# Kernel optimization log

Hardware: AMD Instinct MI355X
Metric: run time of the kernel (lower is better)

## Reference

```python
import jax, jax.numpy as jnp
import numpy as np

INF = 1e9  # large finite sentinel (avoid inf arithmetic in potentials)


def _hungarian(cost):
    """Exact linear sum assignment (Jonker-Volgenant style shortest augmenting
    path, O(N^3)) on a single [N, N] cost matrix. Returns col_ind (int32 [N])
    such that row i is matched to column col_ind[i] with minimal total cost
    (same solution as scipy.optimize.linear_sum_assignment up to ties).
    Column index n is a virtual 'start' column (e-maxx formulation)."""
    n = cost.shape[0]

    def row_body(i, carry):
        u, v, p = carry  # u: row potentials [n]; v: col potentials [n+1]; p[j]: row assigned to col j (-1 free)
        p = p.at[n].set(i)
        state = (u, v, p,
                 jnp.full(n + 1, INF, cost.dtype),   # minv
                 jnp.zeros(n + 1, dtype=bool),       # used
                 jnp.zeros(n + 1, dtype=jnp.int32),  # way (parent col on path)
                 jnp.int32(n))                       # j0 current col

        def cond(st):
            _, _, p_, _, _, _, j0 = st
            return p_[j0] >= 0  # stop when we reach a free column

        def body(st):
            u_, v_, p_, minv, used, way, j0 = st
            used = used.at[j0].set(True)
            i0 = p_[j0]
            cur = cost[i0] - u_[i0] - v_[:n]          # reduced costs of row i0 [n]
            cur = jnp.where(used[:n], INF, cur)
            better = cur < minv[:n]
            minv = minv.at[:n].set(jnp.where(better, cur, minv[:n]))
            way = way.at[:n].set(jnp.where(better, j0, way[:n]))
            masked = jnp.where(used[:n], INF, minv[:n])
            j1 = jnp.argmin(masked).astype(jnp.int32)
            delta = masked[j1]
            # dual update: used cols raise row potential, others shrink minv
            u_ = u_.at[p_].add(jnp.where(used, delta, jnp.zeros((), cost.dtype)))
            v_ = jnp.where(used, v_ - delta, v_)
            minv = jnp.where(used, minv, minv - delta)
            return (u_, v_, p_, minv, used, way, j1)

        u, v, p, _, _, way, j0 = jax.lax.while_loop(cond, body, state)

        # augment along the alternating path back to the virtual column
        def cond2(s):
            j, _ = s
            return j != n

        def body2(s):
            j, p_ = s
            j_prev = way[j]
            return j_prev, p_.at[j].set(p_[j_prev])

        _, p = jax.lax.while_loop(cond2, body2, (j0, p))
        return (u, v, p)

    u0 = jnp.zeros(n, cost.dtype)
    v0 = jnp.zeros(n + 1, cost.dtype)
    p0 = jnp.full(n + 1, -1, dtype=jnp.int32)
    _, _, p = jax.lax.fori_loop(0, n, row_body, (u0, v0, p0))
    # p[j] = row matched to col j  ->  col_ind[row] = j
    col_ind = jnp.zeros(n, jnp.int32).at[p[:n]].set(jnp.arange(n, dtype=jnp.int32))
    return col_ind


def setup_inputs() -> dict:
    key = jax.random.key(0)
    k1, k2 = jax.random.split(key)
    B, N, D = 2048, 24, 256
    slots = jax.random.normal(k1, (B, N, D), dtype=jnp.float32)
    prev_slots = jax.random.normal(k2, (B, N, D), dtype=jnp.float32)
    return {"slots": slots, "prev_slots": prev_slots}


def reference(slots, prev_slots):
    """HungarianPredictor.forward with similarity='cosine': reorder current
    slots to align with prev_slots ordering via optimal 1-1 matching."""
    eps = 1e-12  # torch F.normalize eps
    pn = prev_slots / jnp.maximum(
        jnp.linalg.norm(prev_slots, axis=-1, keepdims=True), eps)
    cn = slots / jnp.maximum(
        jnp.linalg.norm(slots, axis=-1, keepdims=True), eps)
    # cost[b, i, j] = 1 - <prev_i, curr_j>   [B, N, N]
    cost = 1.0 - jnp.einsum('bnd,bmd->bnm', pn, cn)
    col = jax.vmap(_hungarian)(jax.lax.stop_gradient(cost))  # [B, N] int32
    reordered = jax.vmap(lambda s, c: s[c])(slots, col)       # gather per batch
    return reordered
```

## Files before the change

### kernel.cpp

```cpp
#include <hip/hip_runtime.h>

#define N 24
#define D 256
#define DP 260
#define CP 26
#define BLK 256
#define NB 4
#define INFV 1e9f

__global__ __launch_bounds__(BLK) void hungarian_fused(
    const float* __restrict__ slots,
    const float* __restrict__ prev,
    float* __restrict__ out, int B)
{
    __shared__ float sp[N][DP];
    __shared__ float sc[N][DP];
    __shared__ float cost[NB][N][CP];
    __shared__ float inrm[2][N];
    __shared__ int   colw[NB][N];

    const int tid  = threadIdx.x;
    const int lane = tid & 63;
    const int wv   = tid >> 6;
    const int b0   = blockIdx.x * NB;

    for (int m = 0; m < NB; ++m) {
        int b = b0 + m;
        if (b < B) {
            const float4* sb4 = (const float4*)(slots + (size_t)b * N * D);
            const float4* pb4 = (const float4*)(prev  + (size_t)b * N * D);
            #pragma unroll
            for (int r = 0; r < 6; ++r) {
                int i = r * 4 + wv;
                float4 a = sb4[i * 64 + lane];
                float4 c = pb4[i * 64 + lane];
                *(float4*)&sc[i][lane * 4] = a;
                *(float4*)&sp[i][lane * 4] = c;
                float sa = a.x*a.x + a.y*a.y + a.z*a.z + a.w*a.w;
                float sb = c.x*c.x + c.y*c.y + c.z*c.z + c.w*c.w;
                #pragma unroll
                for (int off = 32; off >= 1; off >>= 1) {
                    sa += __shfl_xor(sa, off);
                    sb += __shfl_xor(sb, off);
                }
                if (lane == 0) {
                    inrm[1][i] = 1.0f / fmaxf(sqrtf(sa), 1e-12f);
                    inrm[0][i] = 1.0f / fmaxf(sqrtf(sb), 1e-12f);
                }
            }
        }
        __syncthreads();
        if (b < B && tid < 144) {
            int ti = (tid / 12) * 2;
            int tj = (tid % 12) * 2;
            const float4* p0 = (const float4*)&sp[ti][0];
            const float4* p1 = (const float4*)&sp[ti + 1][0];
            const float4* c0 = (const float4*)&sc[tj][0];
            const float4* c1 = (const float4*)&sc[tj + 1][0];
            float a00 = 0.f, a01 = 0.f, a10 = 0.f, a11 = 0.f;
            int q0 = tid & 63;
            #pragma unroll 4
            for (int k = 0; k < 64; ++k) {
                int q = (q0 + k) & 63;
                float4 x0 = p0[q], x1 = p1[q], y0 = c0[q], y1 = c1[q];
                a00 += x0.x*y0.x + x0.y*y0.y + x0.z*y0.z + x0.w*y0.w;
                a01 += x0.x*y1.x + x0.y*y1.y + x0.z*y1.z + x0.w*y1.w;
                a10 += x1.x*y0.x + x1.y*y0.y + x1.z*y0.z + x1.w*y0.w;
                a11 += x1.x*y1.x + x1.y*y1.y + x1.z*y1.z + x1.w*y1.w;
            }
            float rp0 = inrm[0][ti], rp1 = inrm[0][ti + 1];
            float rc0 = inrm[1][tj], rc1 = inrm[1][tj + 1];
            cost[m][ti][tj]         = 1.0f - a00 * (rp0 * rc0);
            cost[m][ti][tj + 1]     = 1.0f - a01 * (rp0 * rc1);
            cost[m][ti + 1][tj]     = 1.0f - a10 * (rp1 * rc0);
            cost[m][ti + 1][tj + 1] = 1.0f - a11 * (rp1 * rc1);
        }
        __syncthreads();
    }

    const int bw = b0 + wv;
    if (bw < B) {
        const int   jl = lane & 31;
        const float* C = &cost[wv][0][0];
        float u = 0.f;
        float v = 0.f;
        int   p = -1;
        const int jc = (jl < N) ? jl : 0;

        for (int i = 0; i < N; ++i) {
            if (jl == N) p = i;
            float minv = INFV;
            int   way  = 0;
            bool  used = false;
            bool  rowInTree = false;
            int   j0 = N;
            int   i0 = i;

            while (true) {
                used       = used       || (jl == j0);
                rowInTree  = rowInTree  || (jl == i0);
                float u_i0 = __shfl(u, i0, 32);
                float cur  = C[i0 * CP + jc] - u_i0 - v;
                bool  active = (jl < N) && !used;
                if (active && cur < minv) { minv = cur; way = j0; }
                float masked = active ? minv : INFV;

                unsigned k = __float_as_uint(masked);
                k = k ^ ((unsigned)(((int)k) >> 31) | 0x80000000u);
                k = (k & 0xFFFFFFE0u) | (unsigned)jl;
                #pragma unroll
                for (int off = 16; off >= 1; off >>= 1) {
                    unsigned o = __shfl_xor(k, off, 32);
                    k = (o < k) ? o : k;
                }
                int   j1    = (int)(k & 31u);
                float delta = __shfl(masked, j1, 32);

                if (jl < N && rowInTree) u += delta;
                if (jl <= N) {
                    if (used) v -= delta; else minv -= delta;
                }
                j0 = j1;
                i0 = __shfl(p, j0, 32);
                if (i0 < 0) break;
            }

            int j = j0;
            while (j != N) {
                int jp  = __shfl(way, j, 32);
                int pjp = __shfl(p, jp, 32);
                if (jl == j) p = pjp;
                j = jp;
            }
        }
        if (lane < 32 && jl < N) colw[wv][p] = jl;
    }

    if (bw < B) {
        const float4* sg4 = (const float4*)(slots + (size_t)bw * N * D);
        float4*       og4 = (float4*)(out + (size_t)bw * N * D);
        #pragma unroll
        for (int i = 0; i < N; ++i) {
            int c = colw[wv][i];
            og4[i * 64 + lane] = sg4[c * 64 + lane];
        }
    }
}

extern "C" void kernel_launch(void* const* d_in, const int* in_sizes, int n_in,
                              void* d_out, int out_size, void* d_ws, size_t ws_size,
                              hipStream_t stream) {
    const float* slots = (const float*)d_in[0];
    const float* prev  = (const float*)d_in[1];
    float* out = (float*)d_out;
    int B = in_sizes[0] / (N * D);
    int grid = (B + NB - 1) / NB;
    hungarian_fused<<<grid, BLK, 0, stream>>>(slots, prev, out, B);
}
```

Before: 209.6 us.

## Rewrite as per-wave Hungarian with register cost rows, greedy init, DPP reductions

Each wave now builds its own batch's cost matrix. Lanes compute a 3x3 tile of dot products straight from global memory, so the shared staging of slots and prev and the block-wide barriers are gone. The transposed cost is loaded into per-lane registers, and a column-reduction plus greedy initial matching pre-assigns rows, so only the remaining free rows need augmenting paths. The argmin uses DPP row operations and readlane instead of shuffles. This removes LDS traffic and syncs, but the 24-way switch and the greedy init add complexity, and the code relies on a wave-local lgkmcnt wait in place of a barrier for correctness.

Result: faster. 194.5 us (-7.2%).

```diff
diff --git a/kernel.cpp b/kernel.cpp
--- a/kernel.cpp
+++ b/kernel.cpp
@@ -1,149 +1,190 @@
 #include <hip/hip_runtime.h>
-
-#define N 24
-#define D 256
-#define DP 260
-#define CP 26
-#define BLK 256
-#define NB 4
+#include <math.h>
+
+#define N    24
+#define D    256
+#define BLK  256
+#define NB   4
+#define CTS  28
 #define INFV 1e9f
+
+__device__ __forceinline__ int readlane_i(int x, int l) {
+    return __builtin_amdgcn_readlane(x, l);
+}
+__device__ __forceinline__ float readlane_f(float x, int l) {
+    return __uint_as_float((unsigned)__builtin_amdgcn_readlane((int)__float_as_uint(x), l));
+}
+
+__device__ __forceinline__ unsigned wave_min32(unsigned x) {
+    unsigned t;
+    t = (unsigned)__builtin_amdgcn_update_dpp((int)x, (int)x, 0xB1,  0xF, 0xF, false); x = t < x ? t : x;
+    t = (unsigned)__builtin_amdgcn_update_dpp((int)x, (int)x, 0x4E,  0xF, 0xF, false); x = t < x ? t : x;
+    t = (unsigned)__builtin_amdgcn_update_dpp((int)x, (int)x, 0x114, 0xF, 0xF, false); x = t < x ? t : x;
+    t = (unsigned)__builtin_amdgcn_update_dpp((int)x, (int)x, 0x118, 0xF, 0xF, false); x = t < x ? t : x;
+    t = (unsigned)__builtin_amdgcn_update_dpp((int)x, (int)x, 0x142, 0xF, 0xF, false); x = t < x ? t : x;
+    return x;
+}
+
+#define DOT4(a, b) ((a).x*(b).x + (a).y*(b).y + (a).z*(b).z + (a).w*(b).w)
+#define LGKM0() __asm__ volatile("s_waitcnt lgkmcnt(0)" ::: "memory")
 
 __global__ __launch_bounds__(BLK) void hungarian_fused(
     const float* __restrict__ slots,
     const float* __restrict__ prev,
     float* __restrict__ out, int B)
 {
-    __shared__ float sp[N][DP];
-    __shared__ float sc[N][DP];
-    __shared__ float cost[NB][N][CP];
-    __shared__ float inrm[2][N];
-    __shared__ int   colw[NB][N];
+    __shared__ __align__(16) float costT[NB][N][CTS];
+    __shared__ int winner[NB][N];
+    __shared__ int colw[NB][N];
 
     const int tid  = threadIdx.x;
     const int lane = tid & 63;
     const int wv   = tid >> 6;
-    const int b0   = blockIdx.x * NB;
-
-    for (int m = 0; m < NB; ++m) {
-        int b = b0 + m;
-        if (b < B) {
-            const float4* sb4 = (const float4*)(slots + (size_t)b * N * D);
-            const float4* pb4 = (const float4*)(prev  + (size_t)b * N * D);
-            #pragma unroll
-            for (int r = 0; r < 6; ++r) {
-                int i = r * 4 + wv;
-                float4 a = sb4[i * 64 + lane];
-                float4 c = pb4[i * 64 + lane];
-                *(float4*)&sc[i][lane * 4] = a;
-                *(float4*)&sp[i][lane * 4] = c;
-                float sa = a.x*a.x + a.y*a.y + a.z*a.z + a.w*a.w;
-                float sb = c.x*c.x + c.y*c.y + c.z*c.z + c.w*c.w;
-                #pragma unroll
-                for (int off = 32; off >= 1; off >>= 1) {
-                    sa += __shfl_xor(sa, off);
-                    sb += __shfl_xor(sb, off);
-                }
-                if (lane == 0) {
-                    inrm[1][i] = 1.0f / fmaxf(sqrtf(sa), 1e-12f);
-                    inrm[0][i] = 1.0f / fmaxf(sqrtf(sb), 1e-12f);
-                }
+    const int bw   = blockIdx.x * NB + wv;
+    if (bw >= B) return;
+
+    const int rg = lane >> 3;
+    const int cg = lane & 7;
+    const float4* pA = (const float4*)(prev  + (size_t)bw * N * D) + rg * 3 * (D / 4);
+    const float4* pC = (const float4*)(slots + (size_t)bw * N * D) + cg * 3 * (D / 4);
+
+    float s00=0,s01=0,s02=0,s10=0,s11=0,s12=0,s20=0,s21=0,s22=0;
+    float pa0=0,pa1=0,pa2=0,pc0=0,pc1=0,pc2=0;
+    #pragma unroll 2
+    for (int k = 0; k < 64; ++k) {
+        float4 a0 = pA[k], a1 = pA[64+k], a2 = pA[128+k];
+        float4 b0 = pC[k], b1 = pC[64+k], b2 = pC[128+k];
+        s00 += DOT4(a0,b0); s01 += DOT4(a0,b1); s02 += DOT4(a0,b2);
+        s10 += DOT4(a1,b0); s11 += DOT4(a1,b1); s12 += DOT4(a1,b2);
+        s20 += DOT4(a2,b0); s21 += DOT4(a2,b1); s22 += DOT4(a2,b2);
+        pa0 += DOT4(a0,a0); pa1 += DOT4(a1,a1); pa2 += DOT4(a2,a2);
+        pc0 += DOT4(b0,b0); pc1 += DOT4(b1,b1); pc2 += DOT4(b2,b2);
+    }
+    float ira0 = 1.0f / fmaxf(sqrtf(pa0), 1e-12f);
+    float ira1 = 1.0f / fmaxf(sqrtf(pa1), 1e-12f);
+    float ira2 = 1.0f / fmaxf(sqrtf(pa2), 1e-12f);
+    float irc0 = 1.0f / fmaxf(sqrtf(pc0), 1e-12f);
+    float irc1 = 1.0f / fmaxf(sqrtf(pc1), 1e-12f);
+    float irc2 = 1.0f / fmaxf(sqrtf(pc2), 1e-12f);
+
+    {
+        float* ct = &costT[wv][0][0];
+        const int cb = cg * 3, rb = rg * 3;
+        ct[(cb+0)*CTS + rb+0] = 1.0f - s00*ira0*irc0;
+        ct[(cb+1)*CTS + rb+0] = 1.0f - s01*ira0*irc1;
+        ct[(cb+2)*CTS + rb+0] = 1.0f - s02*ira0*irc2;
+        ct[(cb+0)*CTS + rb+1] = 1.0f - s10*ira1*irc0;
+        ct[(cb+1)*CTS + rb+1] = 1.0f - s11*ira1*irc1;
+        ct[(cb+2)*CTS + rb+1] = 1.0f - s12*ira1*irc2;
+        ct[(cb+0)*CTS + rb+2] = 1.0f - s20*ira2*irc0;
+        ct[(cb+1)*CTS + rb+2] = 1.0f - s21*ira2*irc1;
+        ct[(cb+2)*CTS + rb+2] = 1.0f - s22*ira2*irc2;
+    }
+    LGKM0();
+
+    const bool isCol = (lane < N);
+    const int  jj    = isCol ? lane : 0;
+    float cq[24];
+    {
+        const float4* cp4 = (const float4*)&costT[wv][jj][0];
+        #pragma unroll
+        for (int r = 0; r < 6; ++r) {
+            float4 q = cp4[r];
+            cq[r*4+0] = q.x; cq[r*4+1] = q.y; cq[r*4+2] = q.z; cq[r*4+3] = q.w;
+        }
+    }
+
+    float cm = cq[0]; int ri = 0;
+    #pragma unroll
+    for (int i = 1; i < N; ++i) { if (cq[i] < cm) { cm = cq[i]; ri = i; } }
+
+    if (isCol) winner[wv][lane] = -1;
+    LGKM0();
+    if (isCol) winner[wv][ri] = lane;
+    LGKM0();
+    int p = -1;
+    if (isCol && winner[wv][ri] == lane) p = ri;
+    const int widx = isCol ? lane : 0;
+    unsigned long long mm = __ballot(isCol && winner[wv][widx] >= 0);
+    unsigned freeRows = (~(unsigned)mm) & ((1u << N) - 1);
+
+    float uu  = 0.0f;
+    float v   = isCol ? cm : INFV;
+    int   way = -1;
+
+    while (freeRows) {
+        const int f = (int)__builtin_ctz(freeRows);
+        freeRows &= freeRows - 1;
+
+        float minv  = INFV;
+        bool  used  = false;
+        bool  inTree = false;
+        int   s_j0 = -1;
+        int   s_i0 = f;
+        float s_u0 = readlane_f(uu, f);
+        int   j1   = 0;
+
+        while (true) {
+            inTree = inTree || (lane == s_i0);
+            used   = used   || (lane == s_j0);
+
+            float cij;
+            switch (s_i0) {
+                case 0:  cij = cq[0];  break;  case 1:  cij = cq[1];  break;
+                case 2:  cij = cq[2];  break;  case 3:  cij = cq[3];  break;
+                case 4:  cij = cq[4];  break;  case 5:  cij = cq[5];  break;
+                case 6:  cij = cq[6];  break;  case 7:  cij = cq[7];  break;
+                case 8:  cij = cq[8];  break;  case 9:  cij = cq[9];  break;
+                case 10: cij = cq[10]; break;  case 11: cij = cq[11]; break;
+                case 12: cij = cq[12]; break;  case 13: cij = cq[13]; break;
+                case 14: cij = cq[14]; break;  case 15: cij = cq[15]; break;
+                case 16: cij = cq[16]; break;  case 17: cij = cq[17]; break;
+                case 18: cij = cq[18]; break;  case 19: cij = cq[19]; break;
+                case 20: cij = cq[20]; break;  case 21: cij = cq[21]; break;
+                case 22: cij = cq[22]; break;  default: cij = cq[23]; break;
             }
+            float cur = cij - s_u0 - v;
+            bool  act = isCol && !used;
+            if (act && cur < minv) { minv = cur; way = s_j0; }
+            float masked = act ? minv : INFV;
+
+            unsigned key = __float_as_uint(masked);
+            key ^= (unsigned)((int)key >> 31) | 0x80000000u;
+            key  = (key & 0xFFFFFFC0u) | (unsigned)lane;
+            unsigned kmin = (unsigned)readlane_i((int)wave_min32(key), 31);
+            j1 = (int)(kmin & 63u);
+
+            float delta = readlane_f(masked, j1);
+            int   i0n   = readlane_i(p, j1);
+            float u0n   = readlane_f(uu, i0n & 31);
+
+            if (inTree) uu += delta;
+            if (used) v -= delta;
+            else if (act) minv -= delta;
+
+            if (i0n < 0) break;
+            s_j0 = j1; s_i0 = i0n; s_u0 = u0n;
         }
-        __syncthreads();
-        if (b < B && tid < 144) {
-            int ti = (tid / 12) * 2;
-            int tj = (tid % 12) * 2;
-            const float4* p0 = (const float4*)&sp[ti][0];
-            const float4* p1 = (const float4*)&sp[ti + 1][0];
-            const float4* c0 = (const float4*)&sc[tj][0];
-            const float4* c1 = (const float4*)&sc[tj + 1][0];
-            float a00 = 0.f, a01 = 0.f, a10 = 0.f, a11 = 0.f;
-            int q0 = tid & 63;
-            #pragma unroll 4
-            for (int k = 0; k < 64; ++k) {
-                int q = (q0 + k) & 63;
-                float4 x0 = p0[q], x1 = p1[q], y0 = c0[q], y1 = c1[q];
-                a00 += x0.x*y0.x + x0.y*y0.y + x0.z*y0.z + x0.w*y0.w;
-                a01 += x0.x*y1.x + x0.y*y1.y + x0.z*y1.z + x0.w*y1.w;
-                a10 += x1.x*y0.x + x1.y*y0.y + x1.z*y0.z + x1.w*y0.w;
-                a11 += x1.x*y1.x + x1.y*y1.y + x1.z*y1.z + x1.w*y1.w;
-            }
-            float rp0 = inrm[0][ti], rp1 = inrm[0][ti + 1];
-            float rc0 = inrm[1][tj], rc1 = inrm[1][tj + 1];
-            cost[m][ti][tj]         = 1.0f - a00 * (rp0 * rc0);
-            cost[m][ti][tj + 1]     = 1.0f - a01 * (rp0 * rc1);
-            cost[m][ti + 1][tj]     = 1.0f - a10 * (rp1 * rc0);
-            cost[m][ti + 1][tj + 1] = 1.0f - a11 * (rp1 * rc1);
+
+        int jcur = j1;
+        while (true) {
+            int wj   = readlane_i(way, jcur);
+            int pnew = (wj < 0) ? f : readlane_i(p, wj);
+            if (lane == jcur) p = pnew;
+            if (wj < 0) break;
+            jcur = wj;
         }
-        __syncthreads();
-    }
-
-    const int bw = b0 + wv;
-    if (bw < B) {
-        const int   jl = lane & 31;
-        const float* C = &cost[wv][0][0];
-        float u = 0.f;
-        float v = 0.f;
-        int   p = -1;
-        const int jc = (jl < N) ? jl : 0;
-
-        for (int i = 0; i < N; ++i) {
-            if (jl == N) p = i;
-            float minv = INFV;
-            int   way  = 0;
-            bool  used = false;
-            bool  rowInTree = false;
-            int   j0 = N;
-            int   i0 = i;
-
-            while (true) {
-                used       = used       || (jl == j0);
-                rowInTree  = rowInTree  || (jl == i0);
-                float u_i0 = __shfl(u, i0, 32);
-                float cur  = C[i0 * CP + jc] - u_i0 - v;
-                bool  active = (jl < N) && !used;
-                if (active && cur < minv) { minv = cur; way = j0; }
-                float masked = active ? minv : INFV;
-
-                unsigned k = __float_as_uint(masked);
-                k = k ^ ((unsigned)(((int)k) >> 31) | 0x80000000u);
-                k = (k & 0xFFFFFFE0u) | (unsigned)jl;
-                #pragma unroll
-                for (int off = 16; off >= 1; off >>= 1) {
-                    unsigned o = __shfl_xor(k, off, 32);
-                    k = (o < k) ? o : k;
-                }
-                int   j1    = (int)(k & 31u);
-                float delta = __shfl(masked, j1, 32);
-
-                if (jl < N && rowInTree) u += delta;
-                if (jl <= N) {
-                    if (used) v -= delta; else minv -= delta;
-                }
-                j0 = j1;
-                i0 = __shfl(p, j0, 32);
-                if (i0 < 0) break;
-            }
-
-            int j = j0;
-            while (j != N) {
-                int jp  = __shfl(way, j, 32);
-                int pjp = __shfl(p, jp, 32);
-                if (jl == j) p = pjp;
-                j = jp;
-            }
-        }
-        if (lane < 32 && jl < N) colw[wv][p] = jl;
-    }
-
-    if (bw < B) {
-        const float4* sg4 = (const float4*)(slots + (size_t)bw * N * D);
-        float4*       og4 = (float4*)(out + (size_t)bw * N * D);
-        #pragma unroll
-        for (int i = 0; i < N; ++i) {
-            int c = colw[wv][i];
-            og4[i * 64 + lane] = sg4[c * 64 + lane];
-        }
+    }
+
+    if (isCol) colw[wv][p] = lane;
+    LGKM0();
+
+    const float4* sg4 = (const float4*)(slots + (size_t)bw * N * D);
+    float4*       og4 = (float4*)(out + (size_t)bw * N * D);
+    #pragma unroll
+    for (int i = 0; i < N; ++i) {
+        int c = colw[wv][i];
+        og4[i * 64 + lane] = sg4[c * 64 + lane];
     }
 }
 
```
